# Kernel tuning notes

Hardware: AMD Instinct MI355X
Metric: run time of the kernel (lower is better)

## Reference

```python
import jax, jax.numpy as jnp
import numpy as np


def conv2d(x, w, b, stride=1, pad=1):
    y = jax.lax.conv_general_dilated(
        x, w, (stride, stride), [(pad, pad), (pad, pad)],
        dimension_numbers=('NCHW', 'OIHW', 'NCHW'))
    return y + b[None, :, None, None]


def layernorm(x, g, b, eps=1e-5):
    mu = jnp.mean(x, -1, keepdims=True)
    var = jnp.mean((x - mu) ** 2, -1, keepdims=True)
    return (x - mu) * jax.lax.rsqrt(var + eps) * g + b


def setup_inputs() -> dict:
    key = jax.random.key(0)
    ks = iter(jax.random.split(key, 40))
    nf = 4

    def w(shape, scale=0.1):
        return (jax.random.normal(next(ks), shape, jnp.float32) * scale)

    inp = {}
    inp['x'] = jax.random.uniform(next(ks), (8, 3, 512, 512), jnp.float32)
    # curve-estimation convs (channel=4)
    inp['c1_w'], inp['c1_b'] = w((nf, 1, 3, 3)), w((nf,))
    inp['c2_w'], inp['c2_b'] = w((nf, nf, 3, 3)), w((nf,))
    inp['c3_w'], inp['c3_b'] = w((nf, nf, 3, 3)), w((nf,))
    inp['c4_w'], inp['c4_b'] = w((nf, nf, 3, 3)), w((nf,))
    inp['c5_w'], inp['c5_b'] = w((nf, 2 * nf, 3, 3)), w((nf,))
    inp['c6_w'], inp['c6_b'] = w((nf, 2 * nf, 3, 3)), w((nf,))
    inp['c7_w'], inp['c7_b'] = w((1, 2 * nf, 3, 3)), w((1,))
    # global branch: conv 1->16 stride 2, instance norm (affine)
    inp['m_w'], inp['m_b'] = w((16, 1, 3, 3)), w((16,))
    inp['in_g'] = jnp.ones((16,), jnp.float32)
    inp['in_b'] = jnp.zeros((16,), jnp.float32)
    # TF block (d_model=16, nhead=8, dim_ff=128), eval mode (no dropout)
    inp['attn_w'], inp['attn_b'] = w((48, 16)), w((48,))
    inp['out_w'], inp['out_b'] = w((16, 16)), w((16,))
    inp['l1_w'], inp['l1_b'] = w((128, 16)), w((128,))
    inp['l2_w'], inp['l2_b'] = w((16, 128)), w((16,))
    inp['n1_g'] = jnp.ones((16,), jnp.float32)
    inp['n1_b'] = jnp.zeros((16,), jnp.float32)
    inp['n2_g'] = jnp.ones((16,), jnp.float32)
    inp['n2_b'] = jnp.zeros((16,), jnp.float32)
    # F: Conv2d(16, 2, kernel=16, pad=0) over 16x16 -> [B,2,1,1]
    inp['f_w'], inp['f_b'] = w((2, 16, 16, 16)), w((2,))
    return inp


def _forward(x, c1_w, c1_b, c2_w, c2_b, c3_w, c3_b, c4_w, c4_b, c5_w, c5_b,
             c6_w, c6_b, c7_w, c7_b, m_w, m_b, in_g, in_b, attn_w, attn_b,
             out_w, out_b, l1_w, l1_b, l2_w, l2_b, n1_g, n1_b, n2_g, n2_b,
             f_w, f_b):
    relu = jax.nn.relu
    B, _, H, W = x.shape
    red, green, blue = x[:, 0:1], x[:, 1:2], x[:, 2:3]
    v = (red + green + blue) / 3.0  # [B,1,H,W]

    # curve-estimation branch
    x1 = relu(conv2d(v, c1_w, c1_b))
    x2 = relu(conv2d(x1, c2_w, c2_b))
    x3 = relu(conv2d(x2, c3_w, c3_b))
    x4 = relu(conv2d(x3, c4_w, c4_b))
    x5 = relu(conv2d(jnp.concatenate([x3, x4], 1), c5_w, c5_b))
    x6 = relu(conv2d(jnp.concatenate([x2, x5], 1), c6_w, c6_b))
    v_r = jax.nn.sigmoid(conv2d(jnp.concatenate([x1, x6], 1), c7_w, c7_b))

    # where(v>0.999999, 0.999999, .) ; where(v<1e-6, 1e-6, .)  == clip
    v0 = jnp.clip(v, 1e-6, 0.999999)

    # nearest-neighbor resize to 32x32 (torch 'nearest': floor(i * src/dst))
    idx_h = (jnp.arange(32) * H) // 32
    idx_w = (jnp.arange(32) * W) // 32
    v32 = v[:, :, idx_h][:, :, :, idx_w]  # [B,1,32,32]

    # model: conv stride2 -> leaky relu -> instance norm (affine)
    h = conv2d(v32, m_w, m_b, stride=2, pad=1)  # [B,16,16,16]
    h = jnp.where(h >= 0, h, 0.2 * h)
    mu = jnp.mean(h, (2, 3), keepdims=True)
    var = jnp.mean((h - mu) ** 2, (2, 3), keepdims=True)
    v1 = (h - mu) * jax.lax.rsqrt(var + 1e-5)
    v1 = v1 * in_g[None, :, None, None] + in_b[None, :, None, None]

    # TF block on [S=256, B, E=16] tokens, 8 heads of dim 2, eval mode
    bb, cc, ww, hh = v1.shape
    src = v1.reshape(bb, cc, ww * hh).transpose(2, 0, 1)  # [S,B,E]
    S, E, nH = ww * hh, cc, 8
    hd = E // nH
    qkv = src @ attn_w.T + attn_b  # [S,B,3E]
    q, k, vv = jnp.split(qkv, 3, axis=-1)
    q = q.reshape(S, bb, nH, hd)
    k = k.reshape(S, bb, nH, hd)
    vv = vv.reshape(S, bb, nH, hd)
    scores = jnp.einsum('sbhd,tbhd->bhst', q, k) / np.sqrt(hd).astype(np.float32)
    attn = jax.nn.softmax(scores, axis=-1)
    o = jnp.einsum('bhst,tbhd->sbhd', attn, vv).reshape(S, bb, E)
    o = o @ out_w.T + out_b
    src = layernorm(src + o, n1_g, n1_b)
    ff = jax.nn.relu(src @ l1_w.T + l1_b) @ l2_w.T + l2_b
    src = layernorm(src + ff, n2_g, n2_b)
    v5 = src.transpose(1, 2, 0).reshape(bb, cc, ww, hh)

    level = jax.nn.sigmoid(conv2d(v5, f_w, f_b, stride=1, pad=0))[:, :, 0, 0]  # [B,2]

    # per-sample exponent / threshold broadcast (vectorized .item() loop)
    g = (0.1 * level[:, 0] + 0.2)[:, None, None, None]   # [B,1,1,1]
    bcf = (0.04 * level[:, 1] + 0.06)[:, None, None, None]
    r0 = jnp.power(g, v_r)           # g ** r, elementwise per sample
    ev0 = jnp.power(v0, r0)
    L = 400.0 * (bcf - v) ** 3
    L = jnp.where(L < 1e-5, 1e-6, L)
    ev = ev0 - L
    vd = v + 1e-6
    enhance = jnp.concatenate([red / vd * ev, green / vd * ev, blue / vd * ev], 1)
    vvv = jnp.concatenate([v, v, v], 1)
    t = jnp.where(vvv > 0.04, jnp.zeros_like(enhance), enhance)
    return enhance, v_r, t


def reference(x, c1_w, c1_b, c2_w, c2_b, c3_w, c3_b, c4_w, c4_b, c5_w, c5_b,
              c6_w, c6_b, c7_w, c7_b, m_w, m_b, in_g, in_b, attn_w, attn_b,
              out_w, out_b, l1_w, l1_b, l2_w, l2_b, n1_g, n1_b, n2_g, n2_b,
              f_w, f_b):
    return _forward(x, c1_w, c1_b, c2_w, c2_b, c3_w, c3_b, c4_w, c4_b,
                    c5_w, c5_b, c6_w, c6_b, c7_w, c7_b, m_w, m_b, in_g, in_b,
                    attn_w, attn_b, out_w, out_b, l1_w, l1_b, l2_w, l2_b,
                    n1_g, n1_b, n2_g, n2_b, f_w, f_b)
```

## Files before the change

### kernel.cpp

```cpp
#include <hip/hip_runtime.h>
#include <math.h>

#define H 512
#define W 512
#define PLANE (H*W)
#define PLANE4 (PLANE/4)

typedef unsigned int uint;
typedef unsigned short ushort;
typedef _Float16 h2 __attribute__((ext_vector_type(2)));

__device__ __forceinline__ h2 bch2(uint u){ return __builtin_bit_cast(h2, u); }
__device__ __forceinline__ uint pkf16(float a, float b){
  return __builtin_bit_cast(uint, __builtin_amdgcn_cvt_pkrtz(a, b));
}

#define LOADWIN_EVEN(WIN, TL, S, YB, XB) { \
  _Pragma("unroll") for (int r_=0;r_<4;++r_){ \
    uint4 Ua = *(const uint4*)&(TL)[(((YB)+r_)*(S)+(XB))*4]; \
    uint4 Ub = *(const uint4*)&(TL)[(((YB)+r_)*(S)+(XB)+2)*4]; \
    WIN[r_][0][0]=bch2(Ua.x); WIN[r_][0][1]=bch2(Ua.y); \
    WIN[r_][1][0]=bch2(Ua.z); WIN[r_][1][1]=bch2(Ua.w); \
    WIN[r_][2][0]=bch2(Ub.x); WIN[r_][2][1]=bch2(Ub.y); \
    WIN[r_][3][0]=bch2(Ub.z); WIN[r_][3][1]=bch2(Ub.w); } }

#define LOADWIN_ODD(WIN, TL, S, YB, XB) { \
  _Pragma("unroll") for (int r_=0;r_<4;++r_){ \
    uint2 U0 = *(const uint2*)&(TL)[(((YB)+r_)*(S)+(XB))*4]; \
    uint4 U1 = *(const uint4*)&(TL)[(((YB)+r_)*(S)+(XB)+1)*4]; \
    uint2 U2 = *(const uint2*)&(TL)[(((YB)+r_)*(S)+(XB)+3)*4]; \
    WIN[r_][0][0]=bch2(U0.x); WIN[r_][0][1]=bch2(U0.y); \
    WIN[r_][1][0]=bch2(U1.x); WIN[r_][1][1]=bch2(U1.y); \
    WIN[r_][2][0]=bch2(U1.z); WIN[r_][2][1]=bch2(U1.w); \
    WIN[r_][3][0]=bch2(U2.x); WIN[r_][3][1]=bch2(U2.y); } }

#define LOADW(WL, OFF) uint WL[72]; \
  _Pragma("unroll") for (int i_=0;i_<72;++i_) WL[i_] = wpk[(OFF)+i_];

#define DOTACC2(WIN, WL) { \
  _Pragma("unroll") for (int p_=0;p_<2;++p_){ \
    _Pragma("unroll") for (int dy_=0;dy_<3;++dy_){ \
      _Pragma("unroll") for (int dx_=0;dx_<3;++dx_){ \
        h2 aa=WIN[dy_][dx_][p_],   bb=WIN[dy_][dx_+1][p_]; \
        h2 cc=WIN[dy_+1][dx_][p_], dd=WIN[dy_+1][dx_+1][p_]; \
        _Pragma("unroll") for (int co_=0;co_<4;++co_){ \
          h2 wv = bch2((WL)[(co_*2+p_)*9+dy_*3+dx_]); \
          a00[co_]=__builtin_amdgcn_fdot2(aa,wv,a00[co_],false); \
          a01[co_]=__builtin_amdgcn_fdot2(bb,wv,a01[co_],false); \
          a10[co_]=__builtin_amdgcn_fdot2(cc,wv,a10[co_],false); \
          a11[co_]=__builtin_amdgcn_fdot2(dd,wv,a11[co_],false); } } } } }

#define DOTACC1(WIN, WL, PBASE) { \
  _Pragma("unroll") for (int p_=0;p_<2;++p_){ \
    _Pragma("unroll") for (int dy_=0;dy_<3;++dy_){ \
      _Pragma("unroll") for (int dx_=0;dx_<3;++dx_){ \
        h2 wv = bch2((WL)[((PBASE)+p_)*9+dy_*3+dx_]); \
        s00=__builtin_amdgcn_fdot2(WIN[dy_][dx_][p_],  wv,s00,false); \
        s01=__builtin_amdgcn_fdot2(WIN[dy_][dx_+1][p_],wv,s01,false); \
        s10=__builtin_amdgcn_fdot2(WIN[dy_+1][dx_][p_],  wv,s10,false); \
        s11=__builtin_amdgcn_fdot2(WIN[dy_+1][dx_+1][p_],wv,s11,false); } } } }

#define STORE_CORE(TL, S, M00, M01, M10, M11) { \
    float v00[4],v01[4],v10[4],v11[4]; \
    _Pragma("unroll") \
    for (int co_=0;co_<4;++co_){ \
      v00[co_]=(M00)?fmaxf(a00[co_],0.f):0.f; \
      v01[co_]=(M01)?fmaxf(a01[co_],0.f):0.f; \
      v10[co_]=(M10)?fmaxf(a10[co_],0.f):0.f; \
      v11[co_]=(M11)?fmaxf(a11[co_],0.f):0.f; } \
    uint4 rowlo, rowhi; \
    rowlo.x=pkf16(v00[0],v00[1]); rowlo.y=pkf16(v00[2],v00[3]); \
    rowlo.z=pkf16(v01[0],v01[1]); rowlo.w=pkf16(v01[2],v01[3]); \
    rowhi.x=pkf16(v10[0],v10[1]); rowhi.y=pkf16(v10[2],v10[3]); \
    rowhi.z=pkf16(v11[0],v11[1]); rowhi.w=pkf16(v11[2],v11[3]); \
    *(uint4*)&(TL)[(y0*(S)+x0)*4]=rowlo; \
    *(uint4*)&(TL)[((y0+1)*(S)+x0)*4]=rowhi; }

#define STORE_TILE_B(TL, S, GOFF) { \
    bool okr0=(unsigned)(gy0+(GOFF)+y0  )<512u; \
    bool okr1=(unsigned)(gy0+(GOFF)+y0+1)<512u; \
    bool okc0=(unsigned)(gx0+(GOFF)+x0  )<512u; \
    bool okc1=(unsigned)(gx0+(GOFF)+x0+1)<512u; \
    STORE_CORE(TL, S, okr0&okc0, okr0&okc1, okr1&okc0, okr1&okc1) }

template<int S>
__device__ __forceinline__ void accp4sc(const ushort* __restrict__ pl,
    const float* __restrict__ w, int YB, int XB,
    float* a00, float* a01, float* a10, float* a11)
{
  float q[4][4];
  #pragma unroll
  for (int r=0;r<4;++r){
    const ushort* rp = pl + (YB+r)*S + XB;
    h2 p0 = bch2(*(const uint*)rp);
    h2 p1 = bch2(*(const uint*)(rp+2));
    q[r][0]=(float)p0.x; q[r][1]=(float)p0.y; q[r][2]=(float)p1.x; q[r][3]=(float)p1.y;
  }
  #pragma unroll
  for (int dy=0; dy<3; ++dy)
    #pragma unroll
    for (int dx=0; dx<3; ++dx){
      float q00=q[dy][dx], q01=q[dy][dx+1], q10=q[dy+1][dx], q11=q[dy+1][dx+1];
      #pragma unroll
      for (int co=0; co<4; ++co){
        float wv=w[co*9+dy*3+dx];
        a00[co]+=q00*wv; a01[co]+=q01*wv; a10[co]+=q10*wv; a11[co]+=q11*wv;
      }
    }
}

__launch_bounds__(256)
__global__ void k_mnorm(const float* __restrict__ xg, const float* __restrict__ mw,
                        const float* __restrict__ mb, const float* __restrict__ ing,
                        const float* __restrict__ inb, float* __restrict__ src,
                        const float* __restrict__ c2w, const float* __restrict__ c3w,
                        const float* __restrict__ c4w, const float* __restrict__ c5w,
                        const float* __restrict__ c6w, const float* __restrict__ c7w,
                        uint* __restrict__ wpk, float* __restrict__ gbacc){
  if (blockIdx.x == 128){
    if (threadIdx.x < 16) gbacc[threadIdx.x] = 0.f;
    for (int i=threadIdx.x; i<540; i+=256){
      float f0, f1;
      if (i < 504){
        const float* sw; int CIB, rel;
        if      (i<72) { sw=c2w; CIB=0; rel=i;     int co=rel/18,p=(rel%18)/9,tap=rel%9;
                         f0=sw[(co*4+CIB+2*p)*9+tap]; f1=sw[(co*4+CIB+2*p+1)*9+tap]; }
        else if (i<144){ sw=c3w; CIB=0; rel=i-72;  int co=rel/18,p=(rel%18)/9,tap=rel%9;
                         f0=sw[(co*4+CIB+2*p)*9+tap]; f1=sw[(co*4+CIB+2*p+1)*9+tap]; }
        else if (i<216){ sw=c4w; CIB=0; rel=i-144; int co=rel/18,p=(rel%18)/9,tap=rel%9;
                         f0=sw[(co*4+CIB+2*p)*9+tap]; f1=sw[(co*4+CIB+2*p+1)*9+tap]; }
        else if (i<288){ sw=c5w; CIB=0; rel=i-216; int co=rel/18,p=(rel%18)/9,tap=rel%9;
                         f0=sw[(co*8+CIB+2*p)*9+tap]; f1=sw[(co*8+CIB+2*p+1)*9+tap]; }
        else if (i<360){ sw=c5w; CIB=4; rel=i-288; int co=rel/18,p=(rel%18)/9,tap=rel%9;
                         f0=sw[(co*8+CIB+2*p)*9+tap]; f1=sw[(co*8+CIB+2*p+1)*9+tap]; }
        else if (i<432){ sw=c6w; CIB=0; rel=i-360; int co=rel/18,p=(rel%18)/9,tap=rel%9;
                         f0=sw[(co*8+CIB+2*p)*9+tap]; f1=sw[(co*8+CIB+2*p+1)*9+tap]; }
        else           { sw=c6w; CIB=4; rel=i-432; int co=rel/18,p=(rel%18)/9,tap=rel%9;
                         f0=sw[(co*8+CIB+2*p)*9+tap]; f1=sw[(co*8+CIB+2*p+1)*9+tap]; }
      } else {
        int rel=i-504, p=rel/9, tap=rel%9;
        f0=c7w[(2*p)*9+tap]; f1=c7w[(2*p+1)*9+tap];
      }
      wpk[i] = pkf16(f0, f1);
    }
    return;
  }
  int bc = blockIdx.x;
  int b = bc >> 4, c = bc & 15;
  int tid = threadIdx.x;
  int i = tid >> 4, j = tid & 15;
  const float* xp = xg + (size_t)b*3*PLANE;
  float s = mb[c];
  #pragma unroll
  for (int dy=0; dy<3; ++dy){
    int ii = 2*i - 1 + dy;
    if ((unsigned)ii >= 32u) continue;
    #pragma unroll
    for (int dx=0; dx<3; ++dx){
      int jj = 2*j - 1 + dx;
      if ((unsigned)jj >= 32u) continue;
      int off = (ii*16)*W + jj*16;
      float vv = (xp[off] + xp[PLANE+off] + xp[2*PLANE+off]) * (1.f/3.f);
      s += vv * mw[c*9 + dy*3 + dx];
    }
  }
  float h = (s >= 0.f) ? s : 0.2f*s;
  __shared__ float red[256];
  red[tid] = h; __syncthreads();
  for (int off=128; off; off>>=1){ if (tid<off) red[tid]+=red[tid+off]; __syncthreads(); }
  float mu = red[0] * (1.f/256.f);
  __syncthreads();
  float d = h - mu;
  red[tid] = d*d; __syncthreads();
  for (int off=128; off; off>>=1){ if (tid<off) red[tid]+=red[tid+off]; __syncthreads(); }
  float var = red[0] * (1.f/256.f);
  float yv = d * rsqrtf(var + 1e-5f) * ing[c] + inb[c];
  src[(size_t)tid*128 + b*16 + c] = yv;
}

__launch_bounds__(256)
__global__ void k_attn2(const float* __restrict__ src, const float* __restrict__ aw,
                        const float* __restrict__ ab, float* __restrict__ obuf){
  int b = blockIdx.x >> 3, hh = blockIdx.x & 7;
  int t = threadIdx.x;
  __shared__ float kk0[256], kk1[256], vv0[256], vv1[256];
  int tok = t*8 + b;
  float s[16];
  #pragma unroll
  for (int e=0;e<16;++e) s[e] = src[tok*16+e];
  float q0=ab[2*hh], q1=ab[2*hh+1];
  float k0=ab[16+2*hh], k1=ab[16+2*hh+1];
  float v0=ab[32+2*hh], v1=ab[32+2*hh+1];
  #pragma unroll
  for (int e=0;e<16;++e){
    float sv=s[e];
    q0 += sv*aw[(2*hh  )*16+e]; q1 += sv*aw[(2*hh+1)*16+e];
    k0 += sv*aw[(16+2*hh)*16+e]; k1 += sv*aw[(16+2*hh+1)*16+e];
    v0 += sv*aw[(32+2*hh)*16+e]; v1 += sv*aw[(32+2*hh+1)*16+e];
  }
  kk0[t]=k0; kk1[t]=k1; vv0[t]=v0; vv1[t]=v1;
  __syncthreads();
  const float sc = 0.70710678118654752f;
  float l=0.f, a0=0.f, a1=0.f;
  for (int u=0;u<256;++u){
    float p = __expf((q0*kk0[u]+q1*kk1[u])*sc);
    l+=p; a0+=p*vv0[u]; a1+=p*vv1[u];
  }
  float inv=1.f/l;
  obuf[tok*16 + 2*hh]   = a0*inv;
  obuf[tok*16 + 2*hh+1] = a1*inv;
}

__launch_bounds__(64)
__global__ void k_tok(const float* __restrict__ src, const float* __restrict__ obuf,
                      const float* __restrict__ ow, const float* __restrict__ ob,
                      const float* __restrict__ l1w, const float* __restrict__ l1b,
                      const float* __restrict__ l2w, const float* __restrict__ l2b,
                      const float* __restrict__ n1g, const float* __restrict__ n1b,
                      const float* __restrict__ n2g, const float* __restrict__ n2b,
                      const float* __restrict__ fw, float* __restrict__ gbacc){
  int tok = blockIdx.x, tid = threadIdx.x;
  int s = tok >> 3, b = tok & 7;
  __shared__ float shx[16], shy[16], h1[128];
  if (tid < 16){
    float t2 = ob[tid];
    #pragma unroll
    for (int f=0;f<16;++f) t2 += obuf[tok*16+f]*ow[tid*16+f];
    shx[tid] = src[tok*16+tid] + t2;
  }
  __syncthreads();
  if (tid < 16){
    float mu=0.f;
    #pragma unroll
    for (int e=0;e<16;++e) mu+=shx[e];
    mu*=(1.f/16.f);
    float var=0.f;
    #pragma unroll
    for (int e=0;e<16;++e){ float d=shx[e]-mu; var+=d*d; }
    var*=(1.f/16.f);
    shy[tid] = (shx[tid]-mu)*rsqrtf(var+1e-5f)*n1g[tid]+n1b[tid];
  }
  __syncthreads();
  for (int i=tid;i<128;i+=64){
    float u=l1b[i];
    #pragma unroll
    for (int e=0;e<16;++e) u += shy[e]*l1w[i*16+e];
    h1[i]=fmaxf(u,0.f);
  }
  __syncthreads();
  if (tid < 16){
    float x2=l2b[tid];
    for (int jj=0;jj<128;++jj) x2 += h1[jj]*l2w[tid*128+jj];
    shx[tid] = x2 + shy[tid];
  }
  __syncthreads();
  if (tid < 16){
    float mu=0.f;
    #pragma unroll
    for (int e=0;e<16;++e) mu+=shx[e];
    mu*=(1.f/16.f);
    float var=0.f;
    #pragma unroll
    for (int e=0;e<16;++e){ float d=shx[e]-mu; var+=d*d; }
    var*=(1.f/16.f);
    shy[tid]=(shx[tid]-mu)*rsqrtf(var+1e-5f)*n2g[tid]+n2b[tid];
  }
  __syncthreads();
  if (tid < 2){
    float p=0.f;
    #pragma unroll
    for (int c=0;c<16;++c) p += shy[c]*fw[(tid*16+c)*256 + s];
    atomicAdd(&gbacc[b*2+tid], p);
  }
}

__launch_bounds__(512,2)
__global__ void k_megaconv(const float* __restrict__ xg,
    const float* __restrict__ c1w, const float* __restrict__ c1b,
    const float* __restrict__ c2b, const float* __restrict__ c3b,
    const float* __restrict__ c4b, const float* __restrict__ c5b,
    const float* __restrict__ c6b, const float* __restrict__ c7b,
    const uint* __restrict__ wpk, const float* __restrict__ gbr,
    const float* __restrict__ fb,
    float* __restrict__ out)
{
  __shared__ __align__(16) ushort vb[46*46];
  __shared__ __align__(16) ushort t1[44*44*4];
  __shared__ __align__(16) ushort t2[42*42*4];
  __shared__ __align__(16) ushort t3[40*40*4];
  __shared__ __align__(16) ushort t4[38*38*4];
  __shared__ __align__(16) ushort t5[36*36*4];
  __shared__ __align__(16) ushort t6[34*34*4];
  int wg=blockIdx.x, b=wg>>8, t=wg&255, ty=t>>4, tx=t&15;
  int gy0=ty*32, gx0=tx*32, tid=threadIdx.x;
  const float* xp = xg + (size_t)b*3*PLANE;
  const bool interior = (ty>=1)&(ty<=14)&(tx>=1)&(tx<=14);

  if (interior){
    for (int i=tid;i<46*46;i+=512){
      int rr=i/46, cc=i-rr*46;
      int off=(gy0-7+rr)*W + gx0-7+cc;
      float val=(xp[off]+xp[PLANE+off]+xp[2*PLANE+off])*(1.f/3.f);
      _Float16 hv=(_Float16)val;
      vb[i]=*(ushort*)&hv;
    }
  } else {
    for (int i=tid;i<46*46;i+=512){
      int rr=i/46, cc=i-rr*46;
      int gy=gy0-7+rr, gx=gx0-7+cc;
      float val=0.f;
      if (((unsigned)gy<512u)&((unsigned)gx<512u)){
        int off=gy*W+gx;
        val=(xp[off]+xp[PLANE+off]+xp[2*PLANE+off])*(1.f/3.f);
      }
      _Float16 hv=(_Float16)val;
      vb[i]=*(ushort*)&hv;
    }
  }
  __syncthreads();

  if (tid < 484){
    int qy=tid/22, qx=tid-qy*22, y0=2*qy, x0=2*qx;
    float a00[4],a01[4],a10[4],a11[4];
    #pragma unroll
    for (int co=0;co<4;++co){ float bv=c1b[co]; a00[co]=bv;a01[co]=bv;a10[co]=bv;a11[co]=bv; }
    accp4sc<46>(vb, c1w, y0, x0, a00,a01,a10,a11);
    if (interior){ STORE_CORE(t1, 44, true, true, true, true) }
    else         { STORE_TILE_B(t1, 44, -6) }
  }
  __syncthreads();

  if (tid < 441){
    int qy=tid/21, qx=tid-qy*21, y0=2*qy, x0=2*qx;
    float a00[4],a01[4],a10[4],a11[4];
    #pragma unroll
    for (int co=0;co<4;++co){ float bv=c2b[co]; a00[co]=bv;a01[co]=bv;a10[co]=bv;a11[co]=bv; }
    h2 win[4][4][2];
    LOADWIN_EVEN(win, t1, 44, y0, x0)
    LOADW(wl2, 0)
    DOTACC2(win, wl2)
    if (interior){ STORE_CORE(t2, 42, true, true, true, true) }
    else         { STORE_TILE_B(t2, 42, -5) }
  }
  __syncthreads();

  if (tid < 400){
    int qy=tid/20, qx=tid-qy*20, y0=2*qy, x0=2*qx;
    float a00[4],a01[4],a10[4],a11[4];
    #pragma unroll
    for (int co=0;co<4;++co){ float bv=c3b[co]; a00[co]=bv;a01[co]=bv;a10[co]=bv;a11[co]=bv; }
    h2 win[4][4][2];
    LOADWIN_EVEN(win, t2, 42, y0, x0)
    LOADW(wl3, 72)
    DOTACC2(win, wl3)
    if (interior){ STORE_CORE(t3, 40, true, true, true, true) }
    else         { STORE_TILE_B(t3, 40, -4) }
  }
  __syncthreads();

  if (tid < 361){
    int qy=tid/19, qx=tid-qy*19, y0=2*qy, x0=2*qx;
    float a00[4],a01[4],a10[4],a11[4];
    #pragma unroll
    for (int co=0;co<4;++co){ float bv=c4b[co]; a00[co]=bv;a01[co]=bv;a10[co]=bv;a11[co]=bv; }
    h2 win[4][4][2];
    LOADWIN_EVEN(win, t3, 40, y0, x0)
    LOADW(wl4, 144)
    DOTACC2(win, wl4)
    if (interior){ STORE_CORE(t4, 38, true, true, true, true) }
    else         { STORE_TILE_B(t4, 38, -3) }
  }
  __syncthreads();

  if (tid < 324){
    int qy=tid/18, qx=tid-qy*18, y0=2*qy, x0=2*qx;
    float a00[4],a01[4],a10[4],a11[4];
    #pragma unroll
    for (int co=0;co<4;++co){ float bv=c5b[co]; a00[co]=bv;a01[co]=bv;a10[co]=bv;a11[co]=bv; }
    {
      h2 win[4][4][2];
      LOADWIN_ODD(win, t3, 40, y0+1, x0+1)
      LOADW(wlA, 216)
      DOTACC2(win, wlA)
    }
    {
      h2 win[4][4][2];
      LOADWIN_EVEN(win, t4, 38, y0, x0)
      LOADW(wlB, 288)
      DOTACC2(win, wlB)
    }
    if (interior){ STORE_CORE(t5, 36, true, true, true, true) }
    else         { STORE_TILE_B(t5, 36, -2) }
  }
  __syncthreads();

  if (tid < 289){
    int qy=tid/17, qx=tid-qy*17, y0=2*qy, x0=2*qx;
    float a00[4],a01[4],a10[4],a11[4];
    #pragma unroll
    for (int co=0;co<4;++co){ float bv=c6b[co]; a00[co]=bv;a01[co]=bv;a10[co]=bv;a11[co]=bv; }
    {
      h2 win[4][4][2];
      LOADWIN_ODD(win, t2, 42, y0+3, x0+3)
      LOADW(wlA, 360)
      DOTACC2(win, wlA)
    }
    {
      h2 win[4][4][2];
      LOADWIN_EVEN(win, t5, 36, y0, x0)
      LOADW(wlB, 432)
      DOTACC2(win, wlB)
    }
    if (interior){ STORE_CORE(t6, 34, true, true, true, true) }
    else         { STORE_TILE_B(t6, 34, -1) }
  }
  __syncthreads();

  if (tid < 256){
    int qy=tid>>4, qx=tid&15, y0=2*qy, x0=2*qx;
    float bv=c7b[0];
    float s00=bv, s01=bv, s10=bv, s11=bv;
    uint wl7[36];
    #pragma unroll
    for (int i_=0;i_<36;++i_) wl7[i_]=wpk[504+i_];
    {
      h2 win[4][4][2];
      LOADWIN_ODD(win, t1, 44, y0+5, x0+5)
      DOTACC1(win, wl7, 0)
    }
    {
      h2 win[4][4][2];
      LOADWIN_EVEN(win, t6, 34, y0, x0)
      DOTACC1(win, wl7, 2)
    }
    s00 = 1.f/(1.f+__expf(-s00)); s01 = 1.f/(1.f+__expf(-s01));
    s10 = 1.f/(1.f+__expf(-s10)); s11 = 1.f/(1.f+__expf(-s11));
    float* vo = out + 6291456 + (size_t)b*PLANE;
    *(float2*)&vo[(gy0+y0  )*512 + gx0+x0] = make_float2(s00,s01);
    *(float2*)&vo[(gy0+y0+1)*512 + gx0+x0] = make_float2(s10,s11);

    float lev0 = 1.f/(1.f+__expf(-(gbr[b*2+0]+fb[0])));
    float lev1 = 1.f/(1.f+__expf(-(gbr[b*2+1]+fb[1])));
    float gg  = 0.1f*lev0+0.2f;
    float bcf = 0.04f*lev1+0.06f;
    float lg = log2f(gg);
    #pragma unroll
    for (int py=0; py<2; ++py){
      int gy=gy0+y0+py, gx=gx0+x0;
      int off=gy*W+gx;
      float2 R = *(const float2*)&xp[off];
      float2 G = *(const float2*)&xp[PLANE+off];
      float2 B = *(const float2*)&xp[2*PLANE+off];
      float vr0 = py? s10:s00, vr1 = py? s11:s01;
      float2 er,eg,eb,tr,tg,tb;
#define COMP1(RF,GF,BF,VRF,ER,EG,EB,TR,TG,TB) { \
      float vv=(RF+GF+BF)*(1.f/3.f); \
      float v0c=fminf(fmaxf(vv,1e-6f),0.999999f); \
      float r0=exp2f((VRF)*lg); \
      float ev0=exp2f(r0*log2f(v0c)); \
      float dd=bcf-vv; \
      float L=400.f*dd*dd*dd; \
      L=(L<1e-5f)?1e-6f:L; \
      float fac=(ev0-L)/(vv+1e-6f); \
      ER=RF*fac; EG=GF*fac; EB=BF*fac; \
      bool z=vv>0.04f; \
      TR=z?0.f:ER; TG=z?0.f:EG; TB=z?0.f:EB; }
      COMP1(R.x,G.x,B.x,vr0, er.x,eg.x,eb.x, tr.x,tg.x,tb.x)
      COMP1(R.y,G.y,B.y,vr1, er.y,eg.y,eb.y, tr.y,tg.y,tb.y)
#undef COMP1
      *(float2*)&out[(size_t)(b*3+0)*PLANE + off] = er;
      *(float2*)&out[(size_t)(b*3+1)*PLANE + off] = eg;
      *(float2*)&out[(size_t)(b*3+2)*PLANE + off] = eb;
      *(float2*)&out[8388608 + (size_t)(b*3+0)*PLANE + off] = tr;
      *(float2*)&out[8388608 + (size_t)(b*3+1)*PLANE + off] = tg;
      *(float2*)&out[8388608 + (size_t)(b*3+2)*PLANE + off] = tb;
    }
  }
}

extern "C" void kernel_launch(void* const* d_in, const int* in_sizes, int n_in,
                              void* d_out, int out_size, void* d_ws, size_t ws_size,
                              hipStream_t stream) {
  const float* x    = (const float*)d_in[0];
  const float* c1w  = (const float*)d_in[1];  const float* c1b = (const float*)d_in[2];
  const float* c2w  = (const float*)d_in[3];  const float* c2b = (const float*)d_in[4];
  const float* c3w  = (const float*)d_in[5];  const float* c3b = (const float*)d_in[6];
  const float* c4w  = (const float*)d_in[7];  const float* c4b = (const float*)d_in[8];
  const float* c5w  = (const float*)d_in[9];  const float* c5b = (const float*)d_in[10];
  const float* c6w  = (const float*)d_in[11]; const float* c6b = (const float*)d_in[12];
  const float* c7w  = (const float*)d_in[13]; const float* c7b = (const float*)d_in[14];
  const float* mw   = (const float*)d_in[15]; const float* mb  = (const float*)d_in[16];
  const float* ing  = (const float*)d_in[17]; const float* inb = (const float*)d_in[18];
  const float* aw   = (const float*)d_in[19]; const float* ab  = (const float*)d_in[20];
  const float* ow   = (const float*)d_in[21]; const float* ob  = (const float*)d_in[22];
  const float* l1w  = (const float*)d_in[23]; const float* l1b = (const float*)d_in[24];
  const float* l2w  = (const float*)d_in[25]; const float* l2b = (const float*)d_in[26];
  const float* n1g  = (const float*)d_in[27]; const float* n1b = (const float*)d_in[28];
  const float* n2g  = (const float*)d_in[29]; const float* n2b = (const float*)d_in[30];
  const float* fw   = (const float*)d_in[31]; const float* fb  = (const float*)d_in[32];

  uint* wpk = (uint*)d_ws;
  float* gbacc = (float*)(wpk + 1024);
  float* src  = gbacc + 16;
  float* obuf = src + 32768;
  float* out  = (float*)d_out;

  k_mnorm<<<129,256,0,stream>>>(x, mw, mb, ing, inb, src,
                                c2w, c3w, c4w, c5w, c6w, c7w, wpk, gbacc);
  k_attn2<<<64,256,0,stream>>>(src, aw, ab, obuf);
  k_tok<<<2048,64,0,stream>>>(src, obuf, ow, ob, l1w, l1b, l2w, l2b,
                              n1g, n1b, n2g, n2b, fw, gbacc);
  k_megaconv<<<2048,512,0,stream>>>(x, c1w, c1b, c2b, c3b, c4b, c5b, c6b, c7b,
                                    wpk, gbacc, fb, out);
}
```

Measured before the change: 153.7 us.

## Alias LDS buffers in an arena and recompute conv1 for final layer

Replaces the seven separate shared-memory tiles with one aliased arena in which dead intermediate buffers (t1 after stage 2, t3/t4 after later stages) are reused for t6 and t1, shrinking LDS per block. To let t1 be overwritten, the final conv7 no longer reads the t1 skip connection from LDS but recomputes the needed conv1 outputs from the grayscale tile in registers. Launch bounds are raised to 3 blocks per CU to exploit the smaller footprint. This trades extra ALU work and register pressure in the last stage for higher occupancy.

```diff
diff --git a/kernel.cpp b/kernel.cpp
--- a/kernel.cpp
+++ b/kernel.cpp
@@ -274,23 +274,47 @@
   }
 }
 
-__launch_bounds__(512,2)
+#define LOADVB(DST, RR) { \
+  _Pragma("unroll") for (int c_=0;c_<6;++c_) \
+    DST[c_] = (float)(*(const _Float16*)&vbp[((y0+5+(RR)))*46 + x0+5+c_]); }
+
+#define X1R(DST, R0, R1, R2, RBASE) { \
+  _Pragma("unroll") for (int c_=0;c_<4;++c_){ \
+    bool ok_ = interior || (((unsigned)(gy0+y0-1+(RBASE))<512u)&((unsigned)(gx0+x0-1+c_)<512u)); \
+    _Pragma("unroll") for (int co_=0;co_<4;++co_){ \
+      float a_=c1b[co_]; \
+      _Pragma("unroll") for (int dx_=0;dx_<3;++dx_){ \
+        a_ += R0[c_+dx_]*c1w[co_*9+dx_]; \
+        a_ += R1[c_+dx_]*c1w[co_*9+3+dx_]; \
+        a_ += R2[c_+dx_]*c1w[co_*9+6+dx_]; } \
+      DST[c_][co_] = ok_?fmaxf(a_,0.f):0.f; } } }
+
+#define SL7(RL, RH, DYI) { \
+  _Pragma("unroll") for (int dx_=0;dx_<3;++dx_){ \
+    _Pragma("unroll") for (int co_=0;co_<4;++co_){ \
+      float w_=c7w[co_*9+(DYI)*3+dx_]; \
+      s00 += RL[dx_][co_]*w_;   s01 += RL[dx_+1][co_]*w_; \
+      s10 += RH[dx_][co_]*w_;   s11 += RH[dx_+1][co_]*w_; } } }
+
+__launch_bounds__(512,3)
 __global__ void k_megaconv(const float* __restrict__ xg,
     const float* __restrict__ c1w, const float* __restrict__ c1b,
     const float* __restrict__ c2b, const float* __restrict__ c3b,
     const float* __restrict__ c4b, const float* __restrict__ c5b,
     const float* __restrict__ c6b, const float* __restrict__ c7b,
+    const float* __restrict__ c7w,
     const uint* __restrict__ wpk, const float* __restrict__ gbr,
     const float* __restrict__ fb,
     float* __restrict__ out)
 {
-  __shared__ __align__(16) ushort vb[46*46];
-  __shared__ __align__(16) ushort t1[44*44*4];
-  __shared__ __align__(16) ushort t2[42*42*4];
-  __shared__ __align__(16) ushort t3[40*40*4];
-  __shared__ __align__(16) ushort t4[38*38*4];
-  __shared__ __align__(16) ushort t5[36*36*4];
-  __shared__ __align__(16) ushort t6[34*34*4];
+  __shared__ __align__(16) ushort arena[26536];
+  ushort* vbp = arena;
+  ushort* t2  = arena + 2120;
+  ushort* t3  = arena + 9176;
+  ushort* t4  = arena + 15576;
+  ushort* t5  = arena + 21352;
+  ushort* t6  = arena + 9176;
+  ushort* t1  = arena + 15576;
   int wg=blockIdx.x, b=wg>>8, t=wg&255, ty=t>>4, tx=t&15;
   int gy0=ty*32, gx0=tx*32, tid=threadIdx.x;
   const float* xp = xg + (size_t)b*3*PLANE;
@@ -302,7 +326,7 @@
       int off=(gy0-7+rr)*W + gx0-7+cc;
       float val=(xp[off]+xp[PLANE+off]+xp[2*PLANE+off])*(1.f/3.f);
       _Float16 hv=(_Float16)val;
-      vb[i]=*(ushort*)&hv;
+      vbp[i]=*(ushort*)&hv;
     }
   } else {
     for (int i=tid;i<46*46;i+=512){
@@ -314,7 +338,7 @@
         val=(xp[off]+xp[PLANE+off]+xp[2*PLANE+off])*(1.f/3.f);
       }
       _Float16 hv=(_Float16)val;
-      vb[i]=*(ushort*)&hv;
+      vbp[i]=*(ushort*)&hv;
     }
   }
   __syncthreads();
@@ -324,7 +348,7 @@
     float a00[4],a01[4],a10[4],a11[4];
     #pragma unroll
     for (int co=0;co<4;++co){ float bv=c1b[co]; a00[co]=bv;a01[co]=bv;a10[co]=bv;a11[co]=bv; }
-    accp4sc<46>(vb, c1w, y0, x0, a00,a01,a10,a11);
+    accp4sc<46>(vbp, c1w, y0, x0, a00,a01,a10,a11);
     if (interior){ STORE_CORE(t1, 44, true, true, true, true) }
     else         { STORE_TILE_B(t1, 44, -6) }
   }
@@ -425,13 +449,23 @@
     for (int i_=0;i_<36;++i_) wl7[i_]=wpk[504+i_];
     {
       h2 win[4][4][2];
-      LOADWIN_ODD(win, t1, 44, y0+5, x0+5)
-      DOTACC1(win, wl7, 0)
-    }
-    {
-      h2 win[4][4][2];
       LOADWIN_EVEN(win, t6, 34, y0, x0)
       DOTACC1(win, wl7, 2)
+    }
+    {
+      float va[6], vb_[6], vc[6], vd[6];
+      float xr0[4][4], xr1[4][4];
+      LOADVB(va,0) LOADVB(vb_,1) LOADVB(vc,2)
+      X1R(xr0, va, vb_, vc, 0)
+      LOADVB(vd,3)
+      X1R(xr1, vb_, vc, vd, 1)
+      SL7(xr0, xr1, 0)
+      LOADVB(va,4)
+      X1R(xr0, vc, vd, va, 2)
+      SL7(xr1, xr0, 1)
+      LOADVB(vb_,5)
+      X1R(xr1, vd, va, vb_, 3)
+      SL7(xr0, xr1, 2)
     }
     s00 = 1.f/(1.f+__expf(-s00)); s01 = 1.f/(1.f+__expf(-s01));
     s10 = 1.f/(1.f+__expf(-s10)); s11 = 1.f/(1.f+__expf(-s11));
@@ -511,5 +545,5 @@
   k_tok<<<2048,64,0,stream>>>(src, obuf, ow, ob, l1w, l1b, l2w, l2b,
                               n1g, n1b, n2g, n2b, fw, gbacc);
   k_megaconv<<<2048,512,0,stream>>>(x, c1w, c1b, c2b, c3b, c4b, c5b, c6b, c7b,
-                                    wpk, gbacc, fb, out);
-}
+                                    c7w, wpk, gbacc, fb, out);
+}
```

Result: slower. 165.9 us (+8.0%).

## Fuse attention and token MLP kernels into one per-token block kernel

Applied to the files above, without the earlier changes.

Merges the separate attention kernel and token feed-forward kernel into a single kernel with one block per query token, which removes a launch and the intermediate attention-output buffer. Each block recomputes all 256 keys and values for its batch sample in shared memory and reduces the softmax across the block with wave shuffles. This repeats the K/V projection work 256 times per sample in exchange for fewer launches and better parallelism than the old 64-block attention kernel.

```diff
diff --git a/kernel.cpp b/kernel.cpp
--- a/kernel.cpp
+++ b/kernel.cpp
@@ -179,54 +179,85 @@
 }
 
 __launch_bounds__(256)
-__global__ void k_attn2(const float* __restrict__ src, const float* __restrict__ aw,
-                        const float* __restrict__ ab, float* __restrict__ obuf){
-  int b = blockIdx.x >> 3, hh = blockIdx.x & 7;
-  int t = threadIdx.x;
-  __shared__ float kk0[256], kk1[256], vv0[256], vv1[256];
-  int tok = t*8 + b;
-  float s[16];
-  #pragma unroll
-  for (int e=0;e<16;++e) s[e] = src[tok*16+e];
-  float q0=ab[2*hh], q1=ab[2*hh+1];
-  float k0=ab[16+2*hh], k1=ab[16+2*hh+1];
-  float v0=ab[32+2*hh], v1=ab[32+2*hh+1];
-  #pragma unroll
-  for (int e=0;e<16;++e){
-    float sv=s[e];
-    q0 += sv*aw[(2*hh  )*16+e]; q1 += sv*aw[(2*hh+1)*16+e];
-    k0 += sv*aw[(16+2*hh)*16+e]; k1 += sv*aw[(16+2*hh+1)*16+e];
-    v0 += sv*aw[(32+2*hh)*16+e]; v1 += sv*aw[(32+2*hh+1)*16+e];
-  }
-  kk0[t]=k0; kk1[t]=k1; vv0[t]=v0; vv1[t]=v1;
-  __syncthreads();
-  const float sc = 0.70710678118654752f;
-  float l=0.f, a0=0.f, a1=0.f;
-  for (int u=0;u<256;++u){
-    float p = __expf((q0*kk0[u]+q1*kk1[u])*sc);
-    l+=p; a0+=p*vv0[u]; a1+=p*vv1[u];
-  }
-  float inv=1.f/l;
-  obuf[tok*16 + 2*hh]   = a0*inv;
-  obuf[tok*16 + 2*hh+1] = a1*inv;
-}
-
-__launch_bounds__(64)
-__global__ void k_tok(const float* __restrict__ src, const float* __restrict__ obuf,
-                      const float* __restrict__ ow, const float* __restrict__ ob,
-                      const float* __restrict__ l1w, const float* __restrict__ l1b,
-                      const float* __restrict__ l2w, const float* __restrict__ l2b,
-                      const float* __restrict__ n1g, const float* __restrict__ n1b,
-                      const float* __restrict__ n2g, const float* __restrict__ n2b,
-                      const float* __restrict__ fw, float* __restrict__ gbacc){
-  int tok = blockIdx.x, tid = threadIdx.x;
-  int s = tok >> 3, b = tok & 7;
+__global__ void k_smallx(const float* __restrict__ src,
+    const float* __restrict__ aw, const float* __restrict__ ab,
+    const float* __restrict__ ow, const float* __restrict__ ob,
+    const float* __restrict__ l1w, const float* __restrict__ l1b,
+    const float* __restrict__ l2w, const float* __restrict__ l2b,
+    const float* __restrict__ n1g, const float* __restrict__ n1b,
+    const float* __restrict__ n2g, const float* __restrict__ n2b,
+    const float* __restrict__ fw, float* __restrict__ gbacc)
+{
+  int blk = blockIdx.x;
+  int tok_s = blk >> 3, b = blk & 7;
+  int tid = threadIdx.x;
+  __shared__ float kl[256][17];
+  __shared__ float vl[256][17];
+  __shared__ float qs[16];
+  __shared__ float part[4][24];
+  __shared__ float o16[16];
   __shared__ float shx[16], shy[16], h1[128];
+
+  {
+    const float* srow = src + (size_t)(tid*8+b)*16;
+    float su[16];
+    #pragma unroll
+    for (int e=0;e<16;++e) su[e]=srow[e];
+    #pragma unroll
+    for (int o=0;o<16;++o){
+      float kk=ab[16+o], vv=ab[32+o];
+      #pragma unroll
+      for (int e=0;e<16;++e){ kk += su[e]*aw[(16+o)*16+e]; vv += su[e]*aw[(32+o)*16+e]; }
+      kl[tid][o]=kk; vl[tid][o]=vv;
+    }
+    if (tid<16){
+      const float* srs = src + (size_t)(tok_s*8+b)*16;
+      float qq = ab[tid];
+      #pragma unroll
+      for (int e=0;e<16;++e) qq += srs[e]*aw[tid*16+e];
+      qs[tid]=qq;
+    }
+  }
+  __syncthreads();
+
+  {
+    float qv[16];
+    #pragma unroll
+    for (int e=0;e<16;++e) qv[e]=qs[e];
+    const float sc = 0.70710678118654752f;
+    float pr[24];
+    #pragma unroll
+    for (int hh=0;hh<8;++hh){
+      float p = __expf((qv[2*hh]*kl[tid][2*hh]+qv[2*hh+1]*kl[tid][2*hh+1])*sc);
+      pr[3*hh]=p; pr[3*hh+1]=p*vl[tid][2*hh]; pr[3*hh+2]=p*vl[tid][2*hh+1];
+    }
+    #pragma unroll
+    for (int off=32; off; off>>=1){
+      #pragma unroll
+      for (int k=0;k<24;++k) pr[k] += __shfl_down(pr[k], off);
+    }
+    int wv = tid>>6, ln = tid&63;
+    if (ln==0){
+      #pragma unroll
+      for (int k=0;k<24;++k) part[wv][k]=pr[k];
+    }
+  }
+  __syncthreads();
+  if (tid<8){
+    float l=0.f,a0=0.f,a1=0.f;
+    #pragma unroll
+    for (int w=0;w<4;++w){ l+=part[w][3*tid]; a0+=part[w][3*tid+1]; a1+=part[w][3*tid+2]; }
+    float inv=1.f/l;
+    o16[2*tid]=a0*inv; o16[2*tid+1]=a1*inv;
+  }
+  __syncthreads();
+
+  int tok = blk;
   if (tid < 16){
     float t2 = ob[tid];
     #pragma unroll
-    for (int f=0;f<16;++f) t2 += obuf[tok*16+f]*ow[tid*16+f];
-    shx[tid] = src[tok*16+tid] + t2;
+    for (int f=0;f<16;++f) t2 += o16[f]*ow[tid*16+f];
+    shx[tid] = src[(size_t)tok*16+tid] + t2;
   }
   __syncthreads();
   if (tid < 16){
@@ -241,11 +272,11 @@
     shy[tid] = (shx[tid]-mu)*rsqrtf(var+1e-5f)*n1g[tid]+n1b[tid];
   }
   __syncthreads();
-  for (int i=tid;i<128;i+=64){
-    float u=l1b[i];
-    #pragma unroll
-    for (int e=0;e<16;++e) u += shy[e]*l1w[i*16+e];
-    h1[i]=fmaxf(u,0.f);
+  if (tid < 128){
+    float u=l1b[tid];
+    #pragma unroll
+    for (int e=0;e<16;++e) u += shy[e]*l1w[tid*16+e];
+    h1[tid]=fmaxf(u,0.f);
   }
   __syncthreads();
   if (tid < 16){
@@ -269,7 +300,7 @@
   if (tid < 2){
     float p=0.f;
     #pragma unroll
-    for (int c=0;c<16;++c) p += shy[c]*fw[(tid*16+c)*256 + s];
+    for (int c=0;c<16;++c) p += shy[c]*fw[(tid*16+c)*256 + tok_s];
     atomicAdd(&gbacc[b*2+tid], p);
   }
 }
@@ -502,14 +533,12 @@
   uint* wpk = (uint*)d_ws;
   float* gbacc = (float*)(wpk + 1024);
   float* src  = gbacc + 16;
-  float* obuf = src + 32768;
   float* out  = (float*)d_out;
 
   k_mnorm<<<129,256,0,stream>>>(x, mw, mb, ing, inb, src,
                                 c2w, c3w, c4w, c5w, c6w, c7w, wpk, gbacc);
-  k_attn2<<<64,256,0,stream>>>(src, aw, ab, obuf);
-  k_tok<<<2048,64,0,stream>>>(src, obuf, ow, ob, l1w, l1b, l2w, l2b,
-                              n1g, n1b, n2g, n2b, fw, gbacc);
+  k_smallx<<<2048,256,0,stream>>>(src, aw, ab, ow, ob, l1w, l1b, l2w, l2b,
+                                  n1g, n1b, n2g, n2b, fw, gbacc);
   k_megaconv<<<2048,512,0,stream>>>(x, c1w, c1b, c2b, c3b, c4b, c5b, c6b, c7b,
                                     wpk, gbacc, fb, out);
 }
```

After: 156.9 us. 1.02x slower.
